# Optimization experiments

Measured on AMD Instinct MI355X. Metric: run time of the kernel, lower is better.

## Reference

```python
import jax, jax.numpy as jnp
import numpy as np

ALPHA = 0.95
BETA = 0.9

def setup_inputs() -> dict:
    key = jax.random.key(0)
    k1, k2 = jax.random.split(key)
    B, T, I, O = 64, 1000, 512, 256
    inputs = jax.random.normal(k1, (B, T, I), dtype=jnp.float32)
    W = jax.random.normal(k2, (O, I), dtype=jnp.float32) * (1.0 / np.sqrt(I))
    return {"inputs": inputs, "W": W, "nb_steps": T}

def reference(inputs, W, nb_steps):
    B = inputs.shape[0]
    O = W.shape[0]
    # linear projection: h[b,t,o]
    h = jnp.einsum('bti,oi->bto', inputs, W)
    h_t = jnp.swapaxes(h, 0, 1)  # (T, B, O) for scan over time

    def step(carry, ht):
        flt, out = carry
        new_flt = ALPHA * flt + ht
        new_out = BETA * out + flt  # uses OLD flt, matching the torch loop
        return (new_flt, new_out), new_out

    init = (jnp.zeros((B, O), jnp.float32), jnp.zeros((B, O), jnp.float32))
    _, out_rec = jax.lax.scan(step, init, h_t)
    return jnp.swapaxes(out_rec, 0, 1)  # (B, T, O)
```

## Files before the change

kernel.cpp:

```cpp
#include <hip/hip_runtime.h>
#include <stdint.h>


#define ALPHA 0.95f
#define BETA  0.9f

constexpr int Bdim = 64, T = 1000, Idim = 512, Odim = 256;
constexpr int M = Bdim * T;
constexpr int C = 40, L = 25;
constexpr int BO = Bdim * Odim;

typedef short bf16x8 __attribute__((ext_vector_type(8)));
typedef float f32x4  __attribute__((ext_vector_type(4)));

__device__ inline uint32_t pk_bf16(float a, float b) {
  union { float f; uint32_t u; } x, y; x.f = a; y.f = b;
  uint32_t lo = (x.u + 0x7FFFu + ((x.u >> 16) & 1u)) >> 16;
  uint32_t hi = (y.u + 0x7FFFu + ((y.u >> 16) & 1u)) & 0xFFFF0000u;
  return lo | hi;
}
__device__ inline uint16_t f2bf(float a) {
  union { float f; uint32_t u; } x; x.f = a;
  return (uint16_t)((x.u + 0x7FFFu + ((x.u >> 16) & 1u)) >> 16);
}
__device__ inline float bf2f(uint16_t h) {
  union { uint32_t u; float f; } x; x.u = ((uint32_t)h) << 16;
  return x.f;
}

__global__ __launch_bounds__(256) void gemm_h(const float* __restrict__ A,
                                              const float* __restrict__ W,
                                              uint16_t* __restrict__ H) {
  __shared__ uint16_t As[128 * 32];
  __shared__ uint16_t Bs[128 * 32];

  const int tid  = threadIdx.x;
  const int lane = tid & 63;
  const int wave = tid >> 6;
  const int wm   = (wave >> 1) * 64;
  const int wn   = (wave & 1) * 64;
  const int l15  = lane & 15;
  const int quad = lane >> 4;
  const int rm   = blockIdx.x * 128;
  const int cn   = blockIdx.y * 128;

  const int srow = tid >> 2;
  const int sc   = tid & 3;
  int soff[2];
#pragma unroll
  for (int p = 0; p < 2; ++p) {
    int row = p * 64 + srow;
    soff[p] = row * 32 + ((sc ^ (row & 3)) * 8);
  }
  const float* aB0 = A + (size_t)(rm + srow) * Idim + sc * 8;
  const float* aB1 = A + (size_t)(rm + 64 + srow) * Idim + sc * 8;
  const float* bB0 = W + (size_t)(cn + srow) * Idim + sc * 8;
  const float* bB1 = W + (size_t)(cn + 64 + srow) * Idim + sc * 8;

  const int swz = (quad ^ (l15 & 3)) * 8;
  int aoff[4], boff[4];
#pragma unroll
  for (int t = 0; t < 4; ++t) {
    aoff[t] = (wm + t * 16 + l15) * 32 + swz;
    boff[t] = (wn + t * 16 + l15) * 32 + swz;
  }

  f32x4 acc[4][4] = {};

  float4 ra0 = *(const float4*)(aB0),     ra1 = *(const float4*)(aB0 + 4);
  float4 ra2 = *(const float4*)(aB1),     ra3 = *(const float4*)(aB1 + 4);
  float4 rb0 = *(const float4*)(bB0),     rb1 = *(const float4*)(bB0 + 4);
  float4 rb2 = *(const float4*)(bB1),     rb3 = *(const float4*)(bB1 + 4);

  for (int k0 = 0; k0 < Idim; k0 += 32) {
    __syncthreads();
    *(uint4*)&As[soff[0]] = make_uint4(pk_bf16(ra0.x, ra0.y), pk_bf16(ra0.z, ra0.w),
                                       pk_bf16(ra1.x, ra1.y), pk_bf16(ra1.z, ra1.w));
    *(uint4*)&As[soff[1]] = make_uint4(pk_bf16(ra2.x, ra2.y), pk_bf16(ra2.z, ra2.w),
                                       pk_bf16(ra3.x, ra3.y), pk_bf16(ra3.z, ra3.w));
    *(uint4*)&Bs[soff[0]] = make_uint4(pk_bf16(rb0.x, rb0.y), pk_bf16(rb0.z, rb0.w),
                                       pk_bf16(rb1.x, rb1.y), pk_bf16(rb1.z, rb1.w));
    *(uint4*)&Bs[soff[1]] = make_uint4(pk_bf16(rb2.x, rb2.y), pk_bf16(rb2.z, rb2.w),
                                       pk_bf16(rb3.x, rb3.y), pk_bf16(rb3.z, rb3.w));
    if (k0 + 32 < Idim) {
      int kn = k0 + 32;
      ra0 = *(const float4*)(aB0 + kn); ra1 = *(const float4*)(aB0 + kn + 4);
      ra2 = *(const float4*)(aB1 + kn); ra3 = *(const float4*)(aB1 + kn + 4);
      rb0 = *(const float4*)(bB0 + kn); rb1 = *(const float4*)(bB0 + kn + 4);
      rb2 = *(const float4*)(bB1 + kn); rb3 = *(const float4*)(bB1 + kn + 4);
    }
    __syncthreads();

    bf16x8 af[4], bfq[4];
#pragma unroll
    for (int t = 0; t < 4; ++t) af[t]  = *(const bf16x8*)&As[aoff[t]];
#pragma unroll
    for (int t = 0; t < 4; ++t) bfq[t] = *(const bf16x8*)&Bs[boff[t]];
#pragma unroll
    for (int mt = 0; mt < 4; ++mt)
#pragma unroll
      for (int nt = 0; nt < 4; ++nt)
        acc[mt][nt] = __builtin_amdgcn_mfma_f32_16x16x32_bf16(af[mt], bfq[nt], acc[mt][nt], 0, 0, 0);
  }

#pragma unroll
  for (int mt = 0; mt < 4; ++mt)
#pragma unroll
    for (int nt = 0; nt < 4; ++nt)
#pragma unroll
      for (int r = 0; r < 4; ++r) {
        int gm = rm + wm + mt * 16 + quad * 4 + r;
        int gn = cn + wn + nt * 16 + l15;
        H[(size_t)gm * Odim + gn] = f2bf(acc[mt][nt][r]);
      }
}

__global__ __launch_bounds__(256) void scan_local(const uint16_t* __restrict__ H,
                                                  float2* __restrict__ St) {
  const int pair = blockIdx.x * 4 + (threadIdx.x >> 6);
  const int b = pair / C, c = pair % C;
  const int lane = threadIdx.x & 63;
  const ushort4* hp = (const ushort4*)(H + (size_t)(b * T + c * L) * Odim) + lane;
  float f[4] = {}, u[4] = {};
#pragma unroll
  for (int j = 0; j < L; ++j) {
    ushort4 hv = hp[j * 64];
    float h0 = bf2f(hv.x), h1 = bf2f(hv.y), h2 = bf2f(hv.z), h3 = bf2f(hv.w);
    float n0 = BETA * u[0] + f[0]; f[0] = ALPHA * f[0] + h0; u[0] = n0;
    float n1 = BETA * u[1] + f[1]; f[1] = ALPHA * f[1] + h1; u[1] = n1;
    float n2 = BETA * u[2] + f[2]; f[2] = ALPHA * f[2] + h2; u[2] = n2;
    float n3 = BETA * u[3] + f[3]; f[3] = ALPHA * f[3] + h3; u[3] = n3;
  }
  float2* sp = &St[(size_t)c * BO + b * Odim + lane * 4];
#pragma unroll
  for (int i = 0; i < 4; ++i) sp[i] = make_float2(f[i], u[i]);
}

constexpr double dpow(double x, int n) { double r = 1.0; for (int i = 0; i < n; ++i) r *= x; return r; }

__global__ __launch_bounds__(256) void scan_combine(const float2* __restrict__ St,
                                                    float2* __restrict__ Init) {
  constexpr float AL = (float)dpow(0.95, L);
  constexpr float BL = (float)dpow(0.90, L);
  constexpr float WL = (float)((dpow(0.95, L) - dpow(0.90, L)) / (0.95 - 0.90));
  const int i = blockIdx.x * 256 + threadIdx.x;
  float f = 0.f, u = 0.f;
#pragma unroll
  for (int c = 0; c < C; ++c) {
    Init[(size_t)c * BO + i] = make_float2(f, u);
    float2 s = St[(size_t)c * BO + i];
    float nf = AL * f + s.x;
    float nu = BL * u + WL * f + s.y;
    f = nf; u = nu;
  }
}

__global__ __launch_bounds__(256) void scan_final(const uint16_t* __restrict__ H,
                                                  const float2* __restrict__ Init,
                                                  float* __restrict__ Out) {
  const int pair = blockIdx.x * 4 + (threadIdx.x >> 6);
  const int b = pair / C, c = pair % C;
  const int lane = threadIdx.x & 63;
  const size_t base = (size_t)(b * T + c * L) * Odim;
  const ushort4* hp = (const ushort4*)(H + base) + lane;
  float4* op = (float4*)(Out + base) + lane;
  const float2* sp = &Init[(size_t)c * BO + b * Odim + lane * 4];
  float f[4], u[4];
#pragma unroll
  for (int i = 0; i < 4; ++i) { float2 s = sp[i]; f[i] = s.x; u[i] = s.y; }
#pragma unroll
  for (int j = 0; j < L; ++j) {
    ushort4 hv = hp[j * 64];
    float h0 = bf2f(hv.x), h1 = bf2f(hv.y), h2 = bf2f(hv.z), h3 = bf2f(hv.w);
    float4 o4;
    o4.x = BETA * u[0] + f[0]; f[0] = ALPHA * f[0] + h0; u[0] = o4.x;
    o4.y = BETA * u[1] + f[1]; f[1] = ALPHA * f[1] + h1; u[1] = o4.y;
    o4.z = BETA * u[2] + f[2]; f[2] = ALPHA * f[2] + h2; u[2] = o4.z;
    o4.w = BETA * u[3] + f[3]; f[3] = ALPHA * f[3] + h3; u[3] = o4.w;
    op[j * 64] = o4;
  }
}

extern "C" void kernel_launch(void* const* d_in, const int* in_sizes, int n_in,
                              void* d_out, int out_size, void* d_ws, size_t ws_size,
                              hipStream_t stream) {
  const float* A = (const float*)d_in[0];
  const float* W = (const float*)d_in[1];
  float* Out = (float*)d_out;

  uint16_t* H = (uint16_t*)d_ws;
  const size_t hbytes = (size_t)M * Odim * sizeof(uint16_t);
  float2* St   = (float2*)((char*)d_ws + hbytes);
  float2* Init = St + (size_t)C * BO;

  dim3 g1(M / 128, Odim / 128);
  gemm_h<<<g1, 256, 0, stream>>>(A, W, H);
  scan_local<<<Bdim * C / 4, 256, 0, stream>>>(H, St);
  scan_combine<<<BO / 256, 256, 0, stream>>>(St, Init);
  scan_final<<<Bdim * C / 4, 256, 0, stream>>>(H, Init, Out);
}
```

Measured before the change: 250.1 us.

## Keep W slice resident in LDS and stream A directly into MFMA registers

The GEMM now loads a 64x512 bf16 slice of W into LDS once per block, and each wave reads its A rows straight from global memory into registers, converting them to bf16 for the MFMA fragments. This removes the per-k-step LDS staging of A and the two barriers per iteration. The grid is reordered so the four column blocks that share an A row tile are adjacent, which should let L2 absorb the A rereads. In exchange, A is fetched from global memory four times (once per 64-column block), the 64KB LDS footprint limits occupancy, and the direct global loads follow the MFMA fragment pattern, which may coalesce less well.

```diff
diff --git a/kernel.cpp b/kernel.cpp
--- a/kernel.cpp
+++ b/kernel.cpp
@@ -28,79 +28,80 @@
   return x.f;
 }
 
-__global__ __launch_bounds__(256) void gemm_h(const float* __restrict__ A,
-                                              const float* __restrict__ W,
-                                              uint16_t* __restrict__ H) {
-  __shared__ uint16_t As[128 * 32];
-  __shared__ uint16_t Bs[128 * 32];
+__global__ __launch_bounds__(256, 2) void gemm_h(const float* __restrict__ A,
+                                                 const float* __restrict__ W,
+                                                 uint16_t* __restrict__ H) {
+  __shared__ uint16_t Wl[64 * 512];
 
   const int tid  = threadIdx.x;
   const int lane = tid & 63;
   const int wave = tid >> 6;
-  const int wm   = (wave >> 1) * 64;
-  const int wn   = (wave & 1) * 64;
   const int l15  = lane & 15;
   const int quad = lane >> 4;
-  const int rm   = blockIdx.x * 128;
-  const int cn   = blockIdx.y * 128;
-
-  const int srow = tid >> 2;
-  const int sc   = tid & 3;
-  int soff[2];
-#pragma unroll
-  for (int p = 0; p < 2; ++p) {
-    int row = p * 64 + srow;
-    soff[p] = row * 32 + ((sc ^ (row & 3)) * 8);
-  }
-  const float* aB0 = A + (size_t)(rm + srow) * Idim + sc * 8;
-  const float* aB1 = A + (size_t)(rm + 64 + srow) * Idim + sc * 8;
-  const float* bB0 = W + (size_t)(cn + srow) * Idim + sc * 8;
-  const float* bB1 = W + (size_t)(cn + 64 + srow) * Idim + sc * 8;
-
-  const int swz = (quad ^ (l15 & 3)) * 8;
-  int aoff[4], boff[4];
-#pragma unroll
-  for (int t = 0; t < 4; ++t) {
-    aoff[t] = (wm + t * 16 + l15) * 32 + swz;
-    boff[t] = (wn + t * 16 + l15) * 32 + swz;
-  }
+  const int cn   = blockIdx.x * 64;
+  const int rm   = blockIdx.y * 256;
+
+  {
+    const int r  = tid >> 2;
+    const int cb = (tid & 3) * 16;
+    const float* wr = W + (size_t)(cn + r) * Idim;
+#pragma unroll
+    for (int i = 0; i < 16; ++i) {
+      int c = cb + i;
+      float4 lo = *(const float4*)(wr + c * 8);
+      float4 hi = *(const float4*)(wr + c * 8 + 4);
+      *(uint4*)&Wl[r * 512 + ((c ^ (r & 7)) * 8)] =
+          make_uint4(pk_bf16(lo.x, lo.y), pk_bf16(lo.z, lo.w),
+                     pk_bf16(hi.x, hi.y), pk_bf16(hi.z, hi.w));
+    }
+  }
+  __syncthreads();
+
+  const float* ar[4];
+#pragma unroll
+  for (int mt = 0; mt < 4; ++mt)
+    ar[mt] = A + (size_t)(rm + wave * 64 + mt * 16 + l15) * Idim + quad * 8;
 
   f32x4 acc[4][4] = {};
 
-  float4 ra0 = *(const float4*)(aB0),     ra1 = *(const float4*)(aB0 + 4);
-  float4 ra2 = *(const float4*)(aB1),     ra3 = *(const float4*)(aB1 + 4);
-  float4 rb0 = *(const float4*)(bB0),     rb1 = *(const float4*)(bB0 + 4);
-  float4 rb2 = *(const float4*)(bB1),     rb3 = *(const float4*)(bB1 + 4);
-
-  for (int k0 = 0; k0 < Idim; k0 += 32) {
-    __syncthreads();
-    *(uint4*)&As[soff[0]] = make_uint4(pk_bf16(ra0.x, ra0.y), pk_bf16(ra0.z, ra0.w),
-                                       pk_bf16(ra1.x, ra1.y), pk_bf16(ra1.z, ra1.w));
-    *(uint4*)&As[soff[1]] = make_uint4(pk_bf16(ra2.x, ra2.y), pk_bf16(ra2.z, ra2.w),
-                                       pk_bf16(ra3.x, ra3.y), pk_bf16(ra3.z, ra3.w));
-    *(uint4*)&Bs[soff[0]] = make_uint4(pk_bf16(rb0.x, rb0.y), pk_bf16(rb0.z, rb0.w),
-                                       pk_bf16(rb1.x, rb1.y), pk_bf16(rb1.z, rb1.w));
-    *(uint4*)&Bs[soff[1]] = make_uint4(pk_bf16(rb2.x, rb2.y), pk_bf16(rb2.z, rb2.w),
-                                       pk_bf16(rb3.x, rb3.y), pk_bf16(rb3.z, rb3.w));
-    if (k0 + 32 < Idim) {
-      int kn = k0 + 32;
-      ra0 = *(const float4*)(aB0 + kn); ra1 = *(const float4*)(aB0 + kn + 4);
-      ra2 = *(const float4*)(aB1 + kn); ra3 = *(const float4*)(aB1 + kn + 4);
-      rb0 = *(const float4*)(bB0 + kn); rb1 = *(const float4*)(bB0 + kn + 4);
-      rb2 = *(const float4*)(bB1 + kn); rb3 = *(const float4*)(bB1 + kn + 4);
-    }
-    __syncthreads();
-
-    bf16x8 af[4], bfq[4];
-#pragma unroll
-    for (int t = 0; t < 4; ++t) af[t]  = *(const bf16x8*)&As[aoff[t]];
-#pragma unroll
-    for (int t = 0; t < 4; ++t) bfq[t] = *(const bf16x8*)&Bs[boff[t]];
+  float4 cur[4][2];
+#pragma unroll
+  for (int mt = 0; mt < 4; ++mt) {
+    cur[mt][0] = *(const float4*)(ar[mt]);
+    cur[mt][1] = *(const float4*)(ar[mt] + 4);
+  }
+
+#pragma unroll
+  for (int ks = 0; ks < 16; ++ks) {
+    float4 nxt[4][2];
+    if (ks < 15) {
+#pragma unroll
+      for (int mt = 0; mt < 4; ++mt) {
+        nxt[mt][0] = *(const float4*)(ar[mt] + (ks + 1) * 32);
+        nxt[mt][1] = *(const float4*)(ar[mt] + (ks + 1) * 32 + 4);
+      }
+    }
+    bf16x8 bfr[4];
+#pragma unroll
+    for (int nt = 0; nt < 4; ++nt)
+      bfr[nt] = *(const bf16x8*)&Wl[(nt * 16 + l15) * 512 + (((ks * 4 + quad) ^ (l15 & 7)) * 8)];
+    bf16x8 af[4];
+#pragma unroll
+    for (int mt = 0; mt < 4; ++mt) {
+      union { uint4 u; bf16x8 v; } t;
+      t.u = make_uint4(pk_bf16(cur[mt][0].x, cur[mt][0].y), pk_bf16(cur[mt][0].z, cur[mt][0].w),
+                       pk_bf16(cur[mt][1].x, cur[mt][1].y), pk_bf16(cur[mt][1].z, cur[mt][1].w));
+      af[mt] = t.v;
+    }
 #pragma unroll
     for (int mt = 0; mt < 4; ++mt)
 #pragma unroll
       for (int nt = 0; nt < 4; ++nt)
-        acc[mt][nt] = __builtin_amdgcn_mfma_f32_16x16x32_bf16(af[mt], bfq[nt], acc[mt][nt], 0, 0, 0);
+        acc[mt][nt] = __builtin_amdgcn_mfma_f32_16x16x32_bf16(af[mt], bfr[nt], acc[mt][nt], 0, 0, 0);
+    if (ks < 15) {
+#pragma unroll
+      for (int mt = 0; mt < 4; ++mt) { cur[mt][0] = nxt[mt][0]; cur[mt][1] = nxt[mt][1]; }
+    }
   }
 
 #pragma unroll
@@ -109,8 +110,8 @@
     for (int nt = 0; nt < 4; ++nt)
 #pragma unroll
       for (int r = 0; r < 4; ++r) {
-        int gm = rm + wm + mt * 16 + quad * 4 + r;
-        int gn = cn + wn + nt * 16 + l15;
+        int gm = rm + wave * 64 + mt * 16 + quad * 4 + r;
+        int gn = cn + nt * 16 + l15;
         H[(size_t)gm * Odim + gn] = f2bf(acc[mt][nt][r]);
       }
 }
@@ -193,8 +194,7 @@
   float2* St   = (float2*)((char*)d_ws + hbytes);
   float2* Init = St + (size_t)C * BO;
 
-  dim3 g1(M / 128, Odim / 128);
-  gemm_h<<<g1, 256, 0, stream>>>(A, W, H);
+  gemm_h<<<dim3(Odim / 64, M / 256), 256, 0, stream>>>(A, W, H);
   scan_local<<<Bdim * C / 4, 256, 0, stream>>>(H, St);
   scan_combine<<<BO / 256, 256, 0, stream>>>(St, Init);
   scan_final<<<Bdim * C / 4, 256, 0, stream>>>(H, Init, Out);
```

Measured after the change: 274.7 us. +9.8%, slower.
